# Optimization experiments

Hardware: AMD Instinct MI355X
Metric: run time of the kernel (lower is better)

Reference implementation:

```python
import jax, jax.numpy as jnp
import numpy as np
from math import erf, pi, sqrt, exp

D = 2048
TARGET_BITS = 2.5
N_HIGH = 1024  # round(D * frac)
N_LOW = D - N_HIGH
HIGH_MSE_BITS = 2  # ceil(2.5) - 1
LOW_MSE_BITS = 1   # floor(2.5) - 1


def _phi(x):
    return np.exp(-0.5 * x * x) / np.sqrt(2.0 * np.pi)


def _Phi(x):
    return 0.5 * (1.0 + np.vectorize(erf)(x / np.sqrt(2.0)))


def lloyd_max_centroids(bits: int) -> np.ndarray:
    """Lloyd-Max optimal scalar quantizer centroids for N(0,1), 2**bits levels."""
    L = 2 ** bits
    c = np.linspace(-2.0, 2.0, L)
    for _ in range(200):
        b = 0.5 * (c[:-1] + c[1:])                      # decision boundaries
        edges = np.concatenate([[-1e9], b, [1e9]])
        lo, hi = edges[:-1], edges[1:]
        mass = _Phi(hi) - _Phi(lo)
        c = (_phi(lo) - _phi(hi)) / np.maximum(mass, 1e-12)  # conditional mean
    return c.astype(np.float32)


def generate_rotation_matrix(d: int, seed: int) -> np.ndarray:
    rng = np.random.default_rng(seed)
    A = rng.standard_normal((d, d)).astype(np.float64)
    Q, R = np.linalg.qr(A)
    Q = Q * np.sign(np.diag(R))[None, :]
    return Q.astype(np.float32)


def setup_inputs() -> dict:
    key = jax.random.key(0)
    kq, kk = jax.random.split(key)
    queries = jax.random.normal(kq, (1024, D), dtype=jnp.float32)
    keys = jax.random.normal(kk, (4096, D), dtype=jnp.float32)
    Pi = jnp.asarray(generate_rotation_matrix(D, seed=42 + 2000))
    high_centroids = jnp.asarray(lloyd_max_centroids(HIGH_MSE_BITS))  # (4,)
    low_centroids = jnp.asarray(lloyd_max_centroids(LOW_MSE_BITS))    # (2,)
    rng = np.random.default_rng(42)
    S_high = jnp.asarray(rng.standard_normal((N_HIGH, N_HIGH)).astype(np.float32))
    rng2 = np.random.default_rng(42 + 1000)
    S_low = jnp.asarray(rng2.standard_normal((N_LOW, N_LOW)).astype(np.float32))
    return {"queries": queries, "keys": keys, "Pi": Pi,
            "high_centroids": high_centroids, "low_centroids": low_centroids,
            "S_high": S_high, "S_low": S_low}


def _quantize_group(y, centroids, S):
    # nearest-centroid scalar quantization per channel
    idx = jnp.argmin(jnp.abs(y[..., None] - centroids), axis=-1)  # (bk, n_ch)
    y_mse = centroids[idx]
    residual = y - y_mse
    residual_norm = jnp.linalg.norm(residual, axis=-1)            # (bk,)
    signs = jnp.sign(residual @ S.T)                              # (bk, m)
    return y_mse, signs, residual_norm


def _ip_group(q_ch, y_mse, signs, residual_norm, S):
    m = S.shape[0]
    term1 = q_ch @ y_mse.T                                        # (bq, bk)
    # QJL estimator: <q, r> ~ sqrt(pi/2)/m * ||r|| * <S q, sign(S r)>
    term2 = (jnp.sqrt(jnp.float32(pi / 2)) / m) * ((q_ch @ S.T) @ signs.T) * residual_norm[None, :]
    return term1 + term2


def reference(queries, keys, Pi, high_centroids, low_centroids, S_high, S_low):
    # ---- quantize keys ----
    vec_norm = jnp.linalg.norm(keys, axis=-1)                     # (bk,)
    k_n = keys / (vec_norm[:, None] + 1e-8)
    y = k_n @ Pi.T
    yh, yl = y[:, :N_HIGH], y[:, N_HIGH:]
    kmse_h, sg_h, rn_h = _quantize_group(yh, high_centroids, S_high)
    kmse_l, sg_l, rn_l = _quantize_group(yl, low_centroids, S_low)
    # ---- inner product estimate ----
    q_rot = queries @ Pi.T
    qh, ql = q_rot[:, :N_HIGH], q_rot[:, N_HIGH:]
    ip = _ip_group(qh, kmse_h, sg_h, rn_h, S_high) + _ip_group(ql, kmse_l, sg_l, rn_l, S_low)
    return ip * vec_norm[None, :]                                 # (bq, bk)
```

## Files before the change

kernel.cpp:

```cpp
#include <hip/hip_runtime.h>
#include <math.h>

#ifndef M_PI
#define M_PI 3.14159265358979323846
#endif

typedef __attribute__((ext_vector_type(8))) __bf16 bf16x8;
typedef __attribute__((ext_vector_type(4))) float f32x4;
typedef __attribute__((ext_vector_type(2))) float f32x2;
typedef __attribute__((ext_vector_type(8))) unsigned short ushort8;
typedef __attribute__((ext_vector_type(4))) unsigned short ushort4v;

__device__ __forceinline__ unsigned short f2bf(float x) {
    unsigned int u = __float_as_uint(x);
    unsigned int r = (u + 0x7FFFu + ((u >> 16) & 1u)) >> 16;
    return (unsigned short)r;
}

#define PKFMA_L(d, a, b) \
    asm("v_pk_fma_f32 %0, %1, %2, %0 op_sel:[0,0,0] op_sel_hi:[0,1,1]" \
        : "+v"(d) : "v"(a), "v"(b))
#define PKFMA_H(d, a, b) \
    asm("v_pk_fma_f32 %0, %1, %2, %0 op_sel:[1,0,0] op_sel_hi:[1,1,1]" \
        : "+v"(d) : "v"(a), "v"(b))

__global__ __launch_bounds__(256)
void norm_np_k(const float* __restrict__ keys,
               float* __restrict__ den,
               float* __restrict__ vnorm)
{
#pragma clang fp contract(off)
    const int tid = threadIdx.x;
    const int row_l = tid >> 4;
    const int blk = tid & 15;
    const int row = blockIdx.x * 16 + row_l;
    const float* a = keys + (size_t)row * 2048 + blk * 128;

    float r0 = a[0]*a[0], r1 = a[1]*a[1], r2 = a[2]*a[2], r3 = a[3]*a[3];
    float r4 = a[4]*a[4], r5 = a[5]*a[5], r6 = a[6]*a[6], r7 = a[7]*a[7];
    for (int i = 8; i < 128; i += 8) {
        r0 += a[i+0]*a[i+0]; r1 += a[i+1]*a[i+1];
        r2 += a[i+2]*a[i+2]; r3 += a[i+3]*a[i+3];
        r4 += a[i+4]*a[i+4]; r5 += a[i+5]*a[i+5];
        r6 += a[i+6]*a[i+6]; r7 += a[i+7]*a[i+7];
    }
    float bsum = ((r0 + r1) + (r2 + r3)) + ((r4 + r5) + (r6 + r7));

    __shared__ float bs[16][16];
    bs[row_l][blk] = bsum;
    __syncthreads();
    if (blk == 0) {
        const float* b = bs[row_l];
        float q0 = ((b[0] + b[1]) + (b[2] + b[3])) + ((b[4] + b[5]) + (b[6] + b[7]));
        float q1 = ((b[8] + b[9]) + (b[10] + b[11])) + ((b[12] + b[13]) + (b[14] + b[15]));
        float s = q0 + q1;
        float n = (float)sqrt((double)s);
        den[row] = n + 1e-8f;
        vnorm[row] = n;
    }
}

__global__ __launch_bounds__(256)
void kn_k(const float* __restrict__ keys,
          const float* __restrict__ den,
          float* __restrict__ kn)
{
#pragma clang fp contract(off)
    const int idx = (blockIdx.x * 256 + threadIdx.x) * 8;
    const int row = idx >> 11;
    const float d = den[row];
    float4 v0 = *(const float4*)(keys + idx);
    float4 v1 = *(const float4*)(keys + idx + 4);
    v0.x /= d; v0.y /= d; v0.z /= d; v0.w /= d;
    v1.x /= d; v1.y /= d; v1.z /= d; v1.w /= d;
    *(float4*)(kn + idx) = v0;
    *(float4*)(kn + idx + 4) = v1;
}

__global__ __launch_bounds__(256)
void f2bf_k(const float* __restrict__ in, unsigned short* __restrict__ out)
{
    const int i = (blockIdx.x * 256 + threadIdx.x) * 8;
    float4 v0 = *(const float4*)(in + i);
    float4 v1 = *(const float4*)(in + i + 4);
    ushort8 o;
    o[0] = f2bf(v0.x); o[1] = f2bf(v0.y); o[2] = f2bf(v0.z); o[3] = f2bf(v0.w);
    o[4] = f2bf(v1.x); o[5] = f2bf(v1.y); o[6] = f2bf(v1.z); o[7] = f2bf(v1.w);
    *(ushort8*)(out + i) = o;
}

template <int EPI>
__global__ __launch_bounds__(256, 2)
void gemm_dec_k(const float* __restrict__ A, int lda, int a_zoff,
                const float* __restrict__ B0, const float* __restrict__ B1,
                int ldb,
                float* __restrict__ Cf, unsigned short* __restrict__ Cb,
                int c_zoff, int ldc, int K,
                const float* __restrict__ rv0, const float* __restrict__ rv1)
{
#pragma clang fp contract(off)
    __shared__ float As[2][16][132];
    __shared__ float Bs[2][16][132];

    const int z = blockIdx.z;
    const float* Ap = A + (size_t)z * a_zoff;
    const float* Bp = z ? B1 : B0;
    const float* rvp = z ? rv1 : rv0;
    unsigned short* Cbp = (EPI == 1) ? (Cb + (size_t)z * c_zoff) : nullptr;

    const int tid = threadIdx.x;
    const int tr4 = (tid >> 4) * 4;
    const int tc4 = (tid & 15) * 4;
    const int row0 = blockIdx.y * 128;
    const int col0 = blockIdx.x * 128;
    const int sr = tid >> 1;
    const int sk = (tid & 1) * 8;

    const float* ga = Ap + (size_t)(row0 + sr) * lda + sk;
    const float* gb = Bp + (size_t)(col0 + sr) * ldb + sk;

    f32x2 acc[8][4] = {};
    float sa[8], sb[8];

#define LOADSTAGE(off) do { \
    *(float4*)(sa)     = *(const float4*)(ga + (off)); \
    *(float4*)(sa + 4) = *(const float4*)(ga + (off) + 4); \
    *(float4*)(sb)     = *(const float4*)(gb + (off)); \
    *(float4*)(sb + 4) = *(const float4*)(gb + (off) + 4); \
} while (0)

#define STORESTAGE(buf) do { \
    _Pragma("unroll") \
    for (int u = 0; u < 8; ++u) { \
        As[buf][sk + u][sr] = sa[u]; \
        Bs[buf][sk + u][sr] = sb[u]; \
    } \
} while (0)

#define RDFRAG(fa, fb, kk, buf) do { \
    float4 va0 = *(const float4*)&As[buf][kk][tr4]; \
    float4 va1 = *(const float4*)&As[buf][kk][tr4 + 64]; \
    float4 vb0 = *(const float4*)&Bs[buf][kk][tc4]; \
    float4 vb1 = *(const float4*)&Bs[buf][kk][tc4 + 64]; \
    (fa)[0] = (f32x2){va0.x, va0.y}; (fa)[1] = (f32x2){va0.z, va0.w}; \
    (fa)[2] = (f32x2){va1.x, va1.y}; (fa)[3] = (f32x2){va1.z, va1.w}; \
    (fb)[0] = (f32x2){vb0.x, vb0.y}; (fb)[1] = (f32x2){vb0.z, vb0.w}; \
    (fb)[2] = (f32x2){vb1.x, vb1.y}; (fb)[3] = (f32x2){vb1.z, vb1.w}; \
} while (0)

#define FMAS(fa, fb) do { \
    _Pragma("unroll") \
    for (int p = 0; p < 4; ++p) { \
        _Pragma("unroll") \
        for (int q = 0; q < 4; ++q) { \
            PKFMA_L(acc[2*p][q],   (fa)[p], (fb)[q]); \
            PKFMA_H(acc[2*p+1][q], (fa)[p], (fb)[q]); \
        } \
    } \
} while (0)

    LOADSTAGE(0);
    STORESTAGE(0);
    __syncthreads();
    int cur = 0;

    for (int k0 = 0; k0 < K; k0 += 16) {
        const bool more = (k0 + 16 < K);
        if (more) LOADSTAGE(k0 + 16);

        f32x2 fa0[4], fb0[4], fa1[4], fb1[4];
        RDFRAG(fa0, fb0, 0, cur);
        #pragma unroll
        for (int kk = 0; kk < 16; kk += 2) {
            RDFRAG(fa1, fb1, kk + 1, cur);
            FMAS(fa0, fb0);
            if (kk + 2 < 16) RDFRAG(fa0, fb0, kk + 2, cur);
            FMAS(fa1, fb1);
        }

        if (more) STORESTAGE(cur ^ 1);
        __syncthreads();
        cur ^= 1;
    }

    #pragma unroll
    for (int r = 0; r < 8; ++r) {
        const int row = row0 + ((r < 4) ? (tr4 + r) : (64 + tr4 + r - 4));
        if (EPI == 0) {
            float4 lo4 = {acc[r][0].x, acc[r][0].y, acc[r][1].x, acc[r][1].y};
            float4 hi4 = {acc[r][2].x, acc[r][2].y, acc[r][3].x, acc[r][3].y};
            *(float4*)&Cf[(size_t)row * ldc + col0 + tc4]      = lo4;
            *(float4*)&Cf[(size_t)row * ldc + col0 + 64 + tc4] = hi4;
        } else {
            const float s = rvp[row];
            float v[8] = {acc[r][0].x, acc[r][0].y, acc[r][1].x, acc[r][1].y,
                          acc[r][2].x, acc[r][2].y, acc[r][3].x, acc[r][3].y};
            ushort4v o0, o1;
            #pragma unroll
            for (int j = 0; j < 4; ++j) {
                const float t0 = v[j];
                o0[j] = f2bf((t0 > 0.0f) ? s : ((t0 < 0.0f) ? -s : 0.0f));
                const float t1 = v[4 + j];
                o1[j] = f2bf((t1 > 0.0f) ? s : ((t1 < 0.0f) ? -s : 0.0f));
            }
            *(ushort4v*)&Cbp[(size_t)row * ldc + col0 + tc4]      = o0;
            *(ushort4v*)&Cbp[(size_t)row * ldc + col0 + 64 + tc4] = o1;
        }
    }
#undef LOADSTAGE
#undef STORESTAGE
#undef RDFRAG
#undef FMAS
}

__global__ __launch_bounds__(256)
void quant_k(float* __restrict__ Y,
             unsigned short* __restrict__ Bmse,
             const float* __restrict__ ch,
             const float* __restrict__ cl,
             float* __restrict__ sc_h,
             float* __restrict__ sc_l,
             double coefd)
{
#pragma clang fp contract(off)
    const int row = blockIdx.x;
    const int tid = threadIdx.x;
    const int c0 = tid * 8;
    const float h0 = ch[0], h1 = ch[1], h2 = ch[2], h3 = ch[3];
    const float l0 = cl[0], l1 = cl[1];

    float y[8], res[8];
    ushort8 cb;
    *(float4*)(y)     = *(const float4*)(Y + (size_t)row * 2048 + c0);
    *(float4*)(y + 4) = *(const float4*)(Y + (size_t)row * 2048 + c0 + 4);

    const bool high = (tid < 128);
    float ss = 0.0f;
    #pragma unroll
    for (int j = 0; j < 8; ++j) {
        const float v = y[j];
        float cbest;
        if (high) {
            cbest = h0;
            float bd = fabsf(v - h0), dd;
            dd = fabsf(v - h1); if (dd < bd) { bd = dd; cbest = h1; }
            dd = fabsf(v - h2); if (dd < bd) { bd = dd; cbest = h2; }
            dd = fabsf(v - h3); if (dd < bd) { bd = dd; cbest = h3; }
        } else {
            cbest = (fabsf(v - l1) < fabsf(v - l0)) ? l1 : l0;
        }
        res[j] = v - cbest;
        cb[j] = f2bf(cbest);
        ss += res[j] * res[j];
    }
    *(float4*)(Y + (size_t)row * 2048 + c0)     = *(float4*)(res);
    *(float4*)(Y + (size_t)row * 2048 + c0 + 4) = *(float4*)(res + 4);
    *(ushort8*)(Bmse + (size_t)row * 4096 + c0) = cb;

    __shared__ float sm[256];
    sm[tid] = ss;
    __syncthreads();
    for (int o = 64; o > 0; o >>= 1) {
        if ((tid & 127) < o) sm[tid] += sm[tid + o];
        __syncthreads();
    }
    if (tid == 0)   sc_h[row] = (float)(coefd * sqrt((double)sm[0]));
    if (tid == 128) sc_l[row] = (float)(coefd * sqrt((double)sm[128]));
}

template <int EPI>
__global__ __launch_bounds__(256)
void gemm_mfma_k(const unsigned short* __restrict__ A, int lda, int a_zoff,
                 const unsigned short* __restrict__ B0,
                 const unsigned short* __restrict__ B1, int ldb,
                 float* __restrict__ Cf, unsigned short* __restrict__ Cb,
                 int c_zoff, int ldc, int K,
                 const float* __restrict__ colscale)
{
    __shared__ unsigned short As[128][32];
    __shared__ unsigned short Bs[128][32];

    const int z = blockIdx.z;
    const unsigned short* Ap = A + (size_t)z * a_zoff;
    const unsigned short* Bp = z ? B1 : B0;
    unsigned short* Cbp = (EPI == 2) ? (Cb + (size_t)z * c_zoff) : nullptr;

    const int tid = threadIdx.x;
    const int lane = tid & 63;
    const int w = tid >> 6;
    const int wm = w >> 1;
    const int wn = w & 1;
    const int row0 = blockIdx.y * 128;
    const int col0 = blockIdx.x * 128;
    const int frow = lane & 15;
    const int fk = (lane >> 4) * 8;

    const int srow = lane >> 2;
    const int skel = (lane & 3) * 8;

    f32x4 acc[4][4] = {};

    for (int k0 = 0; k0 < K; k0 += 32) {
        __syncthreads();
        #pragma unroll
        for (int c = 0; c < 2; ++c) {
            const int r = w * 32 + c * 16;
            const unsigned short* ga =
                Ap + (size_t)(row0 + r + srow) * lda + k0 + skel;
            const unsigned short* gb =
                Bp + (size_t)(col0 + r + srow) * ldb + k0 + skel;
            __builtin_amdgcn_global_load_lds(
                (const __attribute__((address_space(1))) void*)ga,
                (__attribute__((address_space(3))) void*)&As[r][0], 16, 0, 0);
            __builtin_amdgcn_global_load_lds(
                (const __attribute__((address_space(1))) void*)gb,
                (__attribute__((address_space(3))) void*)&Bs[r][0], 16, 0, 0);
        }
        __syncthreads();

        bf16x8 af[4], bfr[4];
        #pragma unroll
        for (int mi = 0; mi < 4; ++mi)
            af[mi] = *(const bf16x8*)&As[wm * 64 + mi * 16 + frow][fk];
        #pragma unroll
        for (int ni = 0; ni < 4; ++ni)
            bfr[ni] = *(const bf16x8*)&Bs[wn * 64 + ni * 16 + frow][fk];
        #pragma unroll
        for (int mi = 0; mi < 4; ++mi)
            #pragma unroll
            for (int ni = 0; ni < 4; ++ni)
                acc[mi][ni] = __builtin_amdgcn_mfma_f32_16x16x32_bf16(
                    af[mi], bfr[ni], acc[mi][ni], 0, 0, 0);
    }

    const int drow = (lane >> 4) * 4;
    const int dcol = lane & 15;
    #pragma unroll
    for (int mi = 0; mi < 4; ++mi) {
        #pragma unroll
        for (int ni = 0; ni < 4; ++ni) {
            const int c = col0 + wn * 64 + ni * 16 + dcol;
            const float cs = (EPI == 1) ? colscale[c] : 0.0f;
            #pragma unroll
            for (int rg = 0; rg < 4; ++rg) {
                const int r = row0 + wm * 64 + mi * 16 + drow + rg;
                const float v = acc[mi][ni][rg];
                if (EPI == 1) Cf[(size_t)r * ldc + c] = v * cs;
                else          Cbp[(size_t)r * ldc + c] = f2bf(v);
            }
        }
    }
}

extern "C" void kernel_launch(void* const* d_in, const int* in_sizes, int n_in,
                              void* d_out, int out_size, void* d_ws, size_t ws_size,
                              hipStream_t stream)
{
    const float* queries = (const float*)d_in[0];
    const float* keys    = (const float*)d_in[1];
    const float* Pi      = (const float*)d_in[2];
    const float* ch      = (const float*)d_in[3];
    const float* cl      = (const float*)d_in[4];
    const float* S_high  = (const float*)d_in[5];
    const float* S_low   = (const float*)d_in[6];
    float* out = (float*)d_out;

    char* ws = (char*)d_ws;
    float*          kn    = (float*)(ws);
    float*          Y     = (float*)(ws + ((size_t)32 << 20));
    unsigned short* Bbig  = (unsigned short*)(ws + ((size_t)64 << 20));
    unsigned short* Abig  = (unsigned short*)(ws + ((size_t)96 << 20));
    unsigned short* Qb    = (unsigned short*)(ws + ((size_t)104 << 20));
    unsigned short* Pib   = (unsigned short*)(ws + ((size_t)108 << 20));
    unsigned short* Sbh   = (unsigned short*)(ws + ((size_t)116 << 20));
    unsigned short* Sbl   = (unsigned short*)(ws + ((size_t)118 << 20));
    float*          den   = (float*)(ws + ((size_t)120 << 20));
    float*          vnorm = (float*)(ws + ((size_t)120 << 20) + 16384);
    float*          sc_h  = (float*)(ws + ((size_t)120 << 20) + 32768);
    float*          sc_l  = (float*)(ws + ((size_t)120 << 20) + 49152);

    const double coefd = sqrt(M_PI / 2.0) / 1024.0;

    norm_np_k<<<256, 256, 0, stream>>>(keys, den, vnorm);

    kn_k<<<4096, 256, 0, stream>>>(keys, den, kn);

    f2bf_k<<<1024, 256, 0, stream>>>(queries, Qb);
    f2bf_k<<<2048, 256, 0, stream>>>(Pi, Pib);
    f2bf_k<<<512, 256, 0, stream>>>(S_high, Sbh);
    f2bf_k<<<512, 256, 0, stream>>>(S_low, Sbl);

    gemm_dec_k<0><<<dim3(16, 32, 1), 256, 0, stream>>>(
        kn, 2048, 0, Pi, Pi, 2048, Y, nullptr, 0, 2048, 2048, nullptr, nullptr);

    quant_k<<<4096, 256, 0, stream>>>(Y, Bbig, ch, cl, sc_h, sc_l, coefd);

    gemm_dec_k<1><<<dim3(8, 32, 2), 256, 0, stream>>>(
        Y, 2048, 1024, S_high, S_low, 1024,
        nullptr, Bbig + 2048, 1024, 4096, 1024, sc_h, sc_l);

    gemm_mfma_k<2><<<dim3(16, 8, 1), 256, 0, stream>>>(
        Qb, 2048, 0, Pib, Pib, 2048, nullptr, Abig, 0, 4096, 2048, nullptr);
    gemm_mfma_k<2><<<dim3(8, 8, 2), 256, 0, stream>>>(
        Abig, 4096, 1024, Sbh, Sbl, 1024, nullptr, Abig + 2048, 1024, 4096, 1024, nullptr);

    gemm_mfma_k<1><<<dim3(32, 8, 1), 256, 0, stream>>>(
        Abig, 4096, 0, Bbig, Bbig, 4096, out, nullptr, 0, 4096, 4096, vnorm);
}
```

Baseline: 776.8 us.

## Co-schedule FP32 key GEMMs with bf16 query MFMA GEMMs in fused launches

Merges the norm and normalize kernels into one pass. Packs the independent fp32 key-side GEMM blocks and the bf16 MFMA query-side GEMM blocks into single launches (4:1 interleave by block id), so the small query GEMMs fill the GPU alongside the key GEMMs instead of running serially afterward. It also doubles the K-step of the fp32 GEMM to 32 with larger shared buffers, which cuts the number of barriers per K. The cost is a larger shared-memory footprint for the MFMA blocks, which may lower occupancy, and uneven per-block work within each launch.

```diff
diff --git a/kernel.cpp b/kernel.cpp
--- a/kernel.cpp
+++ b/kernel.cpp
@@ -25,9 +25,9 @@
         : "+v"(d) : "v"(a), "v"(b))
 
 __global__ __launch_bounds__(256)
-void norm_np_k(const float* __restrict__ keys,
-               float* __restrict__ den,
-               float* __restrict__ vnorm)
+void norm_kn_k(const float* __restrict__ keys,
+               float* __restrict__ vnorm,
+               float* __restrict__ kn)
 {
 #pragma clang fp contract(off)
     const int tid = threadIdx.x;
@@ -47,6 +47,7 @@
     float bsum = ((r0 + r1) + (r2 + r3)) + ((r4 + r5) + (r6 + r7));
 
     __shared__ float bs[16][16];
+    __shared__ float den16[16];
     bs[row_l][blk] = bsum;
     __syncthreads();
     if (blk == 0) {
@@ -55,26 +56,22 @@
         float q1 = ((b[8] + b[9]) + (b[10] + b[11])) + ((b[12] + b[13]) + (b[14] + b[15]));
         float s = q0 + q1;
         float n = (float)sqrt((double)s);
-        den[row] = n + 1e-8f;
         vnorm[row] = n;
-    }
-}
-
-__global__ __launch_bounds__(256)
-void kn_k(const float* __restrict__ keys,
-          const float* __restrict__ den,
-          float* __restrict__ kn)
-{
-#pragma clang fp contract(off)
-    const int idx = (blockIdx.x * 256 + threadIdx.x) * 8;
-    const int row = idx >> 11;
-    const float d = den[row];
-    float4 v0 = *(const float4*)(keys + idx);
-    float4 v1 = *(const float4*)(keys + idx + 4);
-    v0.x /= d; v0.y /= d; v0.z /= d; v0.w /= d;
-    v1.x /= d; v1.y /= d; v1.z /= d; v1.w /= d;
-    *(float4*)(kn + idx) = v0;
-    *(float4*)(kn + idx + 4) = v1;
+        den16[row_l] = n + 1e-8f;
+    }
+    __syncthreads();
+
+    const float d = den16[row_l];
+    const float* src = keys + (size_t)row * 2048 + blk * 128;
+    float* dst = kn + (size_t)row * 2048 + blk * 128;
+    for (int c = 0; c < 128; c += 8) {
+        float4 v0 = *(const float4*)(src + c);
+        float4 v1 = *(const float4*)(src + c + 4);
+        v0.x /= d; v0.y /= d; v0.z /= d; v0.w /= d;
+        v1.x /= d; v1.y /= d; v1.z /= d; v1.w /= d;
+        *(float4*)(dst + c) = v0;
+        *(float4*)(dst + c + 4) = v1;
+    }
 }
 
 __global__ __launch_bounds__(256)
@@ -90,29 +87,17 @@
 }
 
 template <int EPI>
-__global__ __launch_bounds__(256, 2)
-void gemm_dec_k(const float* __restrict__ A, int lda, int a_zoff,
-                const float* __restrict__ B0, const float* __restrict__ B1,
-                int ldb,
-                float* __restrict__ Cf, unsigned short* __restrict__ Cb,
-                int c_zoff, int ldc, int K,
-                const float* __restrict__ rv0, const float* __restrict__ rv1)
+__device__ __forceinline__
+void dec_body(float (*As)[132], float (*Bs)[132],
+              const float* __restrict__ Ap, int lda,
+              const float* __restrict__ Bp, int ldb,
+              float* __restrict__ Cf, unsigned short* __restrict__ Cb,
+              int ldc, int K, const float* __restrict__ rvp,
+              int row0, int col0, int tid)
 {
 #pragma clang fp contract(off)
-    __shared__ float As[2][16][132];
-    __shared__ float Bs[2][16][132];
-
-    const int z = blockIdx.z;
-    const float* Ap = A + (size_t)z * a_zoff;
-    const float* Bp = z ? B1 : B0;
-    const float* rvp = z ? rv1 : rv0;
-    unsigned short* Cbp = (EPI == 1) ? (Cb + (size_t)z * c_zoff) : nullptr;
-
-    const int tid = threadIdx.x;
     const int tr4 = (tid >> 4) * 4;
     const int tc4 = (tid & 15) * 4;
-    const int row0 = blockIdx.y * 128;
-    const int col0 = blockIdx.x * 128;
     const int sr = tid >> 1;
     const int sk = (tid & 1) * 8;
 
@@ -120,28 +105,34 @@
     const float* gb = Bp + (size_t)(col0 + sr) * ldb + sk;
 
     f32x2 acc[8][4] = {};
-    float sa[8], sb[8];
+    float sa[16], sb[16];
 
 #define LOADSTAGE(off) do { \
-    *(float4*)(sa)     = *(const float4*)(ga + (off)); \
-    *(float4*)(sa + 4) = *(const float4*)(ga + (off) + 4); \
-    *(float4*)(sb)     = *(const float4*)(gb + (off)); \
-    *(float4*)(sb + 4) = *(const float4*)(gb + (off) + 4); \
+    *(float4*)(sa)      = *(const float4*)(ga + (off)); \
+    *(float4*)(sa + 4)  = *(const float4*)(ga + (off) + 4); \
+    *(float4*)(sa + 8)  = *(const float4*)(ga + (off) + 16); \
+    *(float4*)(sa + 12) = *(const float4*)(ga + (off) + 20); \
+    *(float4*)(sb)      = *(const float4*)(gb + (off)); \
+    *(float4*)(sb + 4)  = *(const float4*)(gb + (off) + 4); \
+    *(float4*)(sb + 8)  = *(const float4*)(gb + (off) + 16); \
+    *(float4*)(sb + 12) = *(const float4*)(gb + (off) + 20); \
 } while (0)
 
-#define STORESTAGE(buf) do { \
+#define STORESTAGE(bo) do { \
     _Pragma("unroll") \
     for (int u = 0; u < 8; ++u) { \
-        As[buf][sk + u][sr] = sa[u]; \
-        Bs[buf][sk + u][sr] = sb[u]; \
+        As[(bo) + sk + u][sr]      = sa[u]; \
+        As[(bo) + 16 + sk + u][sr] = sa[8 + u]; \
+        Bs[(bo) + sk + u][sr]      = sb[u]; \
+        Bs[(bo) + 16 + sk + u][sr] = sb[8 + u]; \
     } \
 } while (0)
 
-#define RDFRAG(fa, fb, kk, buf) do { \
-    float4 va0 = *(const float4*)&As[buf][kk][tr4]; \
-    float4 va1 = *(const float4*)&As[buf][kk][tr4 + 64]; \
-    float4 vb0 = *(const float4*)&Bs[buf][kk][tc4]; \
-    float4 vb1 = *(const float4*)&Bs[buf][kk][tc4 + 64]; \
+#define RDFRAG(fa, fb, kk, bo) do { \
+    float4 va0 = *(const float4*)&As[(bo) + (kk)][tr4]; \
+    float4 va1 = *(const float4*)&As[(bo) + (kk)][tr4 + 64]; \
+    float4 vb0 = *(const float4*)&Bs[(bo) + (kk)][tc4]; \
+    float4 vb1 = *(const float4*)&Bs[(bo) + (kk)][tc4 + 64]; \
     (fa)[0] = (f32x2){va0.x, va0.y}; (fa)[1] = (f32x2){va0.z, va0.w}; \
     (fa)[2] = (f32x2){va1.x, va1.y}; (fa)[3] = (f32x2){va1.z, va1.w}; \
     (fb)[0] = (f32x2){vb0.x, vb0.y}; (fb)[1] = (f32x2){vb0.z, vb0.w}; \
@@ -164,21 +155,22 @@
     __syncthreads();
     int cur = 0;
 
-    for (int k0 = 0; k0 < K; k0 += 16) {
-        const bool more = (k0 + 16 < K);
-        if (more) LOADSTAGE(k0 + 16);
-
+    for (int k0 = 0; k0 < K; k0 += 32) {
+        const bool more = (k0 + 32 < K);
+        if (more) LOADSTAGE(k0 + 32);
+
+        const int bo = cur * 32;
         f32x2 fa0[4], fb0[4], fa1[4], fb1[4];
-        RDFRAG(fa0, fb0, 0, cur);
-        #pragma unroll
-        for (int kk = 0; kk < 16; kk += 2) {
-            RDFRAG(fa1, fb1, kk + 1, cur);
+        RDFRAG(fa0, fb0, 0, bo);
+        #pragma unroll
+        for (int kk = 0; kk < 32; kk += 2) {
+            RDFRAG(fa1, fb1, kk + 1, bo);
             FMAS(fa0, fb0);
-            if (kk + 2 < 16) RDFRAG(fa0, fb0, kk + 2, cur);
+            if (kk + 2 < 32) RDFRAG(fa0, fb0, kk + 2, bo);
             FMAS(fa1, fb1);
         }
 
-        if (more) STORESTAGE(cur ^ 1);
+        if (more) STORESTAGE((cur ^ 1) * 32);
         __syncthreads();
         cur ^= 1;
     }
@@ -203,14 +195,158 @@
                 const float t1 = v[4 + j];
                 o1[j] = f2bf((t1 > 0.0f) ? s : ((t1 < 0.0f) ? -s : 0.0f));
             }
-            *(ushort4v*)&Cbp[(size_t)row * ldc + col0 + tc4]      = o0;
-            *(ushort4v*)&Cbp[(size_t)row * ldc + col0 + 64 + tc4] = o1;
+            *(ushort4v*)&Cb[(size_t)row * ldc + col0 + tc4]      = o0;
+            *(ushort4v*)&Cb[(size_t)row * ldc + col0 + 64 + tc4] = o1;
         }
     }
 #undef LOADSTAGE
 #undef STORESTAGE
 #undef RDFRAG
 #undef FMAS
+}
+
+template <int EPI>
+__device__ __forceinline__
+void mfma_body(unsigned short (*As)[32], unsigned short (*Bs)[32],
+               const unsigned short* __restrict__ Ap, int lda,
+               const unsigned short* __restrict__ Bp, int ldb,
+               float* __restrict__ Cf, unsigned short* __restrict__ Cb,
+               int ldc, int K, const float* __restrict__ colscale,
+               int row0, int col0, int tid)
+{
+    const int lane = tid & 63;
+    const int w = tid >> 6;
+    const int wm = w >> 1;
+    const int wn = w & 1;
+    const int frow = lane & 15;
+    const int fk = (lane >> 4) * 8;
+    const int srow = lane >> 2;
+    const int skel = (lane & 3) * 8;
+
+    f32x4 acc[4][4] = {};
+
+    for (int k0 = 0; k0 < K; k0 += 32) {
+        __syncthreads();
+        #pragma unroll
+        for (int c = 0; c < 2; ++c) {
+            const int r = w * 32 + c * 16;
+            const unsigned short* ga =
+                Ap + (size_t)(row0 + r + srow) * lda + k0 + skel;
+            const unsigned short* gb =
+                Bp + (size_t)(col0 + r + srow) * ldb + k0 + skel;
+            __builtin_amdgcn_global_load_lds(
+                (const __attribute__((address_space(1))) void*)ga,
+                (__attribute__((address_space(3))) void*)&As[r][0], 16, 0, 0);
+            __builtin_amdgcn_global_load_lds(
+                (const __attribute__((address_space(1))) void*)gb,
+                (__attribute__((address_space(3))) void*)&Bs[r][0], 16, 0, 0);
+        }
+        __syncthreads();
+
+        bf16x8 af[4], bfr[4];
+        #pragma unroll
+        for (int mi = 0; mi < 4; ++mi)
+            af[mi] = *(const bf16x8*)&As[wm * 64 + mi * 16 + frow][fk];
+        #pragma unroll
+        for (int ni = 0; ni < 4; ++ni)
+            bfr[ni] = *(const bf16x8*)&Bs[wn * 64 + ni * 16 + frow][fk];
+        #pragma unroll
+        for (int mi = 0; mi < 4; ++mi)
+            #pragma unroll
+            for (int ni = 0; ni < 4; ++ni)
+                acc[mi][ni] = __builtin_amdgcn_mfma_f32_16x16x32_bf16(
+                    af[mi], bfr[ni], acc[mi][ni], 0, 0, 0);
+    }
+
+    const int drow = (lane >> 4) * 4;
+    const int dcol = lane & 15;
+    #pragma unroll
+    for (int mi = 0; mi < 4; ++mi) {
+        #pragma unroll
+        for (int ni = 0; ni < 4; ++ni) {
+            const int c = col0 + wn * 64 + ni * 16 + dcol;
+            const float cs = (EPI == 1) ? colscale[c] : 0.0f;
+            #pragma unroll
+            for (int rg = 0; rg < 4; ++rg) {
+                const int r = row0 + wm * 64 + mi * 16 + drow + rg;
+                const float v = acc[mi][ni][rg];
+                if (EPI == 1) Cf[(size_t)r * ldc + c] = v * cs;
+                else          Cb[(size_t)r * ldc + c] = f2bf(v);
+            }
+        }
+    }
+}
+
+__global__ __launch_bounds__(256, 2)
+void fusedA_k(const float* __restrict__ kn, const float* __restrict__ Pi,
+              float* __restrict__ Y,
+              const unsigned short* __restrict__ Qb,
+              const unsigned short* __restrict__ Pib,
+              unsigned short* __restrict__ Abig)
+{
+    __shared__ __align__(16) char smem[67584];
+    const int bid = blockIdx.x;
+    const int tid = threadIdx.x;
+    if (bid % 5 == 4) {
+        const int mb = bid / 5;
+        const int bx = mb & 15, by = mb >> 4;
+        mfma_body<2>((unsigned short(*)[32])smem,
+                     (unsigned short(*)[32])(smem + 8192),
+                     Qb, 2048, Pib, 2048, nullptr, Abig, 4096, 2048,
+                     nullptr, by * 128, bx * 128, tid);
+    } else {
+        const int db = bid - (bid + 1) / 5;
+        const int bx = db & 15, by = db >> 4;
+        dec_body<0>((float(*)[132])smem, (float(*)[132])(smem + 33792),
+                    kn, 2048, Pi, 2048, Y, nullptr, 2048, 2048,
+                    nullptr, by * 128, bx * 128, tid);
+    }
+}
+
+__global__ __launch_bounds__(256, 2)
+void fusedB_k(const float* __restrict__ Y,
+              const float* __restrict__ S_high, const float* __restrict__ S_low,
+              unsigned short* __restrict__ Bbig,
+              const float* __restrict__ sc_h, const float* __restrict__ sc_l,
+              const unsigned short* __restrict__ Sbh,
+              const unsigned short* __restrict__ Sbl,
+              unsigned short* __restrict__ Abig)
+{
+    __shared__ __align__(16) char smem[67584];
+    const int bid = blockIdx.x;
+    const int tid = threadIdx.x;
+    if (bid % 5 == 4) {
+        const int mb = bid / 5;
+        const int zz = mb >> 6;
+        const int r = mb & 63;
+        const int bx = r & 7, by = r >> 3;
+        mfma_body<2>((unsigned short(*)[32])smem,
+                     (unsigned short(*)[32])(smem + 8192),
+                     Abig + zz * 1024, 4096, (zz ? Sbl : Sbh), 1024,
+                     nullptr, Abig + 2048 + zz * 1024, 4096, 1024,
+                     nullptr, by * 128, bx * 128, tid);
+    } else {
+        const int db = bid - (bid + 1) / 5;
+        const int zz = db >> 8;
+        const int r = db & 255;
+        const int bx = r & 7, by = r >> 3;
+        dec_body<1>((float(*)[132])smem, (float(*)[132])(smem + 33792),
+                    Y + zz * 1024, 2048, (zz ? S_low : S_high), 1024,
+                    nullptr, Bbig + 2048 + zz * 1024, 4096, 1024,
+                    (zz ? sc_l : sc_h), by * 128, bx * 128, tid);
+    }
+}
+
+__global__ __launch_bounds__(256)
+void final_mfma_k(const unsigned short* __restrict__ Abig,
+                  const unsigned short* __restrict__ Bbig,
+                  float* __restrict__ out,
+                  const float* __restrict__ vnorm)
+{
+    __shared__ unsigned short As[128][32];
+    __shared__ unsigned short Bs[128][32];
+    mfma_body<1>(As, Bs, Abig, 4096, Bbig, 4096, out, nullptr, 4096, 4096,
+                 vnorm, blockIdx.y * 128, blockIdx.x * 128, threadIdx.x);
 }
 
 __global__ __launch_bounds__(256)
@@ -268,90 +404,6 @@
     if (tid == 128) sc_l[row] = (float)(coefd * sqrt((double)sm[128]));
 }
 
-template <int EPI>
-__global__ __launch_bounds__(256)
-void gemm_mfma_k(const unsigned short* __restrict__ A, int lda, int a_zoff,
-                 const unsigned short* __restrict__ B0,
-                 const unsigned short* __restrict__ B1, int ldb,
-                 float* __restrict__ Cf, unsigned short* __restrict__ Cb,
-                 int c_zoff, int ldc, int K,
-                 const float* __restrict__ colscale)
-{
-    __shared__ unsigned short As[128][32];
-    __shared__ unsigned short Bs[128][32];
-
-    const int z = blockIdx.z;
-    const unsigned short* Ap = A + (size_t)z * a_zoff;
-    const unsigned short* Bp = z ? B1 : B0;
-    unsigned short* Cbp = (EPI == 2) ? (Cb + (size_t)z * c_zoff) : nullptr;
-
-    const int tid = threadIdx.x;
-    const int lane = tid & 63;
-    const int w = tid >> 6;
-    const int wm = w >> 1;
-    const int wn = w & 1;
-    const int row0 = blockIdx.y * 128;
-    const int col0 = blockIdx.x * 128;
-    const int frow = lane & 15;
-    const int fk = (lane >> 4) * 8;
-
-    const int srow = lane >> 2;
-    const int skel = (lane & 3) * 8;
-
-    f32x4 acc[4][4] = {};
-
-    for (int k0 = 0; k0 < K; k0 += 32) {
-        __syncthreads();
-        #pragma unroll
-        for (int c = 0; c < 2; ++c) {
-            const int r = w * 32 + c * 16;
-            const unsigned short* ga =
-                Ap + (size_t)(row0 + r + srow) * lda + k0 + skel;
-            const unsigned short* gb =
-                Bp + (size_t)(col0 + r + srow) * ldb + k0 + skel;
-            __builtin_amdgcn_global_load_lds(
-                (const __attribute__((address_space(1))) void*)ga,
-                (__attribute__((address_space(3))) void*)&As[r][0], 16, 0, 0);
-            __builtin_amdgcn_global_load_lds(
-                (const __attribute__((address_space(1))) void*)gb,
-                (__attribute__((address_space(3))) void*)&Bs[r][0], 16, 0, 0);
-        }
-        __syncthreads();
-
-        bf16x8 af[4], bfr[4];
-        #pragma unroll
-        for (int mi = 0; mi < 4; ++mi)
-            af[mi] = *(const bf16x8*)&As[wm * 64 + mi * 16 + frow][fk];
-        #pragma unroll
-        for (int ni = 0; ni < 4; ++ni)
-            bfr[ni] = *(const bf16x8*)&Bs[wn * 64 + ni * 16 + frow][fk];
-        #pragma unroll
-        for (int mi = 0; mi < 4; ++mi)
-            #pragma unroll
-            for (int ni = 0; ni < 4; ++ni)
-                acc[mi][ni] = __builtin_amdgcn_mfma_f32_16x16x32_bf16(
-                    af[mi], bfr[ni], acc[mi][ni], 0, 0, 0);
-    }
-
-    const int drow = (lane >> 4) * 4;
-    const int dcol = lane & 15;
-    #pragma unroll
-    for (int mi = 0; mi < 4; ++mi) {
-        #pragma unroll
-        for (int ni = 0; ni < 4; ++ni) {
-            const int c = col0 + wn * 64 + ni * 16 + dcol;
-            const float cs = (EPI == 1) ? colscale[c] : 0.0f;
-            #pragma unroll
-            for (int rg = 0; rg < 4; ++rg) {
-                const int r = row0 + wm * 64 + mi * 16 + drow + rg;
-                const float v = acc[mi][ni][rg];
-                if (EPI == 1) Cf[(size_t)r * ldc + c] = v * cs;
-                else          Cbp[(size_t)r * ldc + c] = f2bf(v);
-            }
-        }
-    }
-}
-
 extern "C" void kernel_launch(void* const* d_in, const int* in_sizes, int n_in,
                               void* d_out, int out_size, void* d_ws, size_t ws_size,
                               hipStream_t stream)
@@ -374,36 +426,25 @@
     unsigned short* Pib   = (unsigned short*)(ws + ((size_t)108 << 20));
     unsigned short* Sbh   = (unsigned short*)(ws + ((size_t)116 << 20));
     unsigned short* Sbl   = (unsigned short*)(ws + ((size_t)118 << 20));
-    float*          den   = (float*)(ws + ((size_t)120 << 20));
-    float*          vnorm = (float*)(ws + ((size_t)120 << 20) + 16384);
-    float*          sc_h  = (float*)(ws + ((size_t)120 << 20) + 32768);
-    float*          sc_l  = (float*)(ws + ((size_t)120 << 20) + 49152);
+    float*          vnorm = (float*)(ws + ((size_t)120 << 20));
+    float*          sc_h  = (float*)(ws + ((size_t)120 << 20) + 16384);
+    float*          sc_l  = (float*)(ws + ((size_t)120 << 20) + 32768);
 
     const double coefd = sqrt(M_PI / 2.0) / 1024.0;
 
-    norm_np_k<<<256, 256, 0, stream>>>(keys, den, vnorm);
-
-    kn_k<<<4096, 256, 0, stream>>>(keys, den, kn);
+    norm_kn_k<<<256, 256, 0, stream>>>(keys, vnorm, kn);
 
     f2bf_k<<<1024, 256, 0, stream>>>(queries, Qb);
     f2bf_k<<<2048, 256, 0, stream>>>(Pi, Pib);
     f2bf_k<<<512, 256, 0, stream>>>(S_high, Sbh);
     f2bf_k<<<512, 256, 0, stream>>>(S_low, Sbl);
 
-    gemm_dec_k<0><<<dim3(16, 32, 1), 256, 0, stream>>>(
-        kn, 2048, 0, Pi, Pi, 2048, Y, nullptr, 0, 2048, 2048, nullptr, nullptr);
+    fusedA_k<<<640, 256, 0, stream>>>(kn, Pi, Y, Qb, Pib, Abig);
 
     quant_k<<<4096, 256, 0, stream>>>(Y, Bbig, ch, cl, sc_h, sc_l, coefd);
 
-    gemm_dec_k<1><<<dim3(8, 32, 2), 256, 0, stream>>>(
-        Y, 2048, 1024, S_high, S_low, 1024,
-        nullptr, Bbig + 2048, 1024, 4096, 1024, sc_h, sc_l);
-
-    gemm_mfma_k<2><<<dim3(16, 8, 1), 256, 0, stream>>>(
-        Qb, 2048, 0, Pib, Pib, 2048, nullptr, Abig, 0, 4096, 2048, nullptr);
-    gemm_mfma_k<2><<<dim3(8, 8, 2), 256, 0, stream>>>(
-        Abig, 4096, 1024, Sbh, Sbl, 1024, nullptr, Abig + 2048, 1024, 4096, 1024, nullptr);
-
-    gemm_mfma_k<1><<<dim3(32, 8, 1), 256, 0, stream>>>(
-        Abig, 4096, 0, Bbig, Bbig, 4096, out, nullptr, 0, 4096, 4096, vnorm);
-}
+    fusedB_k<<<640, 256, 0, stream>>>(Y, S_high, S_low, Bbig, sc_h, sc_l,
+                                      Sbh, Sbl, Abig);
+
+    final_mfma_k<<<dim3(32, 8), 256, 0, stream>>>(Abig, Bbig, out, vnorm);
+}
```

New measurement: 902.1 us. +16.1%, slower.
